# Performance work log

Hardware: AMD Instinct MI355X
Metric: run time of the kernel (lower is better)

The kernel has to match this reference:

```python
import jax, jax.numpy as jnp
from jax import lax
import numpy as np

EPS = 1e-5

def _bn(x, g, b):
    # training-mode BatchNorm2d: batch stats over (N, H, W), biased variance
    m = x.mean(axis=(0, 2, 3), keepdims=True)
    v = x.var(axis=(0, 2, 3), keepdims=True)
    return g[None, :, None, None] * (x - m) * lax.rsqrt(v + EPS) + b[None, :, None, None]

def _conv(x, w, b, stride, pad):
    y = lax.conv_general_dilated(x, w, (stride, stride), ((pad, pad), (pad, pad)),
                                 dimension_numbers=('NCHW', 'OIHW', 'NCHW'))
    return y + b[None, :, None, None]

def _convT(x, w, b):
    # torch ConvTranspose2d(k=4, stride=2, pad=1): equivalent to lhs-dilated conv
    # with spatially flipped kernel and padding k-1-pad = 2. w layout: (Cin, Cout, kh, kw)
    wf = jnp.transpose(w[:, :, ::-1, ::-1], (1, 0, 2, 3))  # -> (Cout, Cin, 4, 4)
    y = lax.conv_general_dilated(x, wf, (1, 1), ((2, 2), (2, 2)), lhs_dilation=(2, 2),
                                 dimension_numbers=('NCHW', 'OIHW', 'NCHW'))
    return y + b[None, :, None, None]

def setup_inputs() -> dict:
    key = jax.random.key(0)
    ks = jax.random.split(key, 8)
    s = 0.05
    inp = {
        'x':   jax.random.normal(ks[0], (32, 1, 256, 256), jnp.float32),
        'w1':  jax.random.normal(ks[1], (16, 1, 4, 4), jnp.float32) * s,
        'b1':  jnp.zeros((16,), jnp.float32),
        'g1':  jnp.ones((16,), jnp.float32),
        'be1': jnp.zeros((16,), jnp.float32),
        'w2':  jax.random.normal(ks[2], (32, 16, 4, 4), jnp.float32) * s,
        'b2':  jnp.zeros((32,), jnp.float32),
        'g2':  jnp.ones((32,), jnp.float32),
        'be2': jnp.zeros((32,), jnp.float32),
        'w3':  jax.random.normal(ks[3], (32, 32, 1, 1), jnp.float32) * s,
        'b3':  jnp.zeros((32,), jnp.float32),
        'g3':  jnp.ones((32,), jnp.float32),
        'be3': jnp.zeros((32,), jnp.float32),
        'emb': jax.random.normal(ks[4], (512, 32), jnp.float32) / 512.0,
        'dw1': jax.random.normal(ks[5], (32, 32, 1, 1), jnp.float32) * s,
        'db1': jnp.zeros((32,), jnp.float32),
        'dg1': jnp.ones((32,), jnp.float32),
        'dbe1': jnp.zeros((32,), jnp.float32),
        'dtw1': jax.random.normal(ks[6], (32, 16, 4, 4), jnp.float32) * s,
        'dtb1': jnp.zeros((16,), jnp.float32),
        'dg2': jnp.ones((16,), jnp.float32),
        'dbe2': jnp.zeros((16,), jnp.float32),
        'dtw2': jax.random.normal(ks[7], (16, 30, 4, 4), jnp.float32) * s,
        'dtb2': jnp.zeros((30,), jnp.float32),
    }
    return inp

def reference(x, w1, b1, g1, be1, w2, b2, g2, be2, w3, b3, g3, be3, emb,
              dw1, db1, dg1, dbe1, dtw1, dtb1, dg2, dbe2, dtw2, dtb2):
    # --- encoder ---
    h = jax.nn.relu(_bn(_conv(x, w1, b1, 2, 1), g1, be1))
    h = jax.nn.relu(_bn(_conv(h, w2, b2, 2, 1), g2, be2))
    z_e_x = _bn(_conv(h, w3, b3, 1, 0), g3, be3)            # (N, C, H, W)
    N, C, H, W = z_e_x.shape
    # --- VQ: matmul-based squared distance (same argmin as broadcast-subtract-sum) ---
    zt = jnp.transpose(z_e_x, (0, 2, 3, 1)).reshape(-1, C)  # (N*H*W, C)
    d = (jnp.sum(zt * zt, axis=1, keepdims=True)
         - 2.0 * zt @ emb.T
         + jnp.sum(emb * emb, axis=1)[None, :])             # (N*H*W, K)
    latents = jnp.argmin(d, axis=1).reshape(N, H, W)        # first-min index, like torch
    z_q_x = jnp.transpose(emb[latents], (0, 3, 1, 2))       # (N, C, H, W)
    # --- decoder ---
    h = jax.nn.relu(_bn(_conv(z_q_x, dw1, db1, 1, 0), dg1, dbe1))
    h = jax.nn.relu(_bn(_convT(h, dtw1, dtb1), dg2, dbe2))
    x_tilde = _convT(h, dtw2, dtb2)                          # (N, 30, 4H, 4W)
    return x_tilde, z_e_x, z_q_x, latents
```

## Files before the change

### kernel.cpp

```cpp
#include <hip/hip_runtime.h>
#include <hip/hip_bf16.h>

#define WS_SUMS  0
#define WS_W1T   4096
#define WS_W2T   8192
#define WS_W3T   40960
#define WS_DW1T  45056
#define WS_DT1T  49152
#define WS_DT2T  81920
#define WS_E2F   114688
#define WS_Y1    1048576
#define WS_Y5    1048576

#define SUM1 0
#define SUM2 512
#define SUM3 1024
#define SUM4 1536
#define SUM5 2048

#define OUT_XT 0
#define OUT_ZE 62914560
#define OUT_ZQ 67108864
#define OUT_LT 71303168

#define DO_Y2 0
#define DO_Y3 16777216
#define DO_Y4 33554432

__device__ __forceinline__ double ae9_wsumd(double v){
  #pragma unroll
  for (int off = 32; off; off >>= 1) v += __shfl_xor(v, off);
  return v;
}

template<int C>
__device__ __forceinline__ void ae9_statsf(const float* a, double* red, double* gsum){
  const int lane = threadIdx.x & 63, wid = threadIdx.x >> 6;
  #pragma unroll
  for (int c = 0; c < C; ++c){
    double av = (double)a[c];
    double s = ae9_wsumd(av);
    double q = ae9_wsumd(av*av);
    if (lane == 0){ red[(wid*C + c)*2] = s; red[(wid*C + c)*2 + 1] = q; }
  }
  __syncthreads();
  if ((int)threadIdx.x < C){
    double s = 0.0, q = 0.0;
    #pragma unroll
    for (int wv = 0; wv < 4; ++wv){ s += red[(wv*C + threadIdx.x)*2]; q += red[(wv*C + threadIdx.x)*2 + 1]; }
    atomicAdd(&gsum[2*threadIdx.x],     s);
    atomicAdd(&gsum[2*threadIdx.x + 1], q);
  }
}

template<int C>
__device__ __forceinline__ void ae9_statsf2(const float* a0, const float* a1, double* red, double* gsum){
  const int lane = threadIdx.x & 63, wid = threadIdx.x >> 6;
  #pragma unroll
  for (int c = 0; c < C; ++c){
    double v0 = (double)a0[c], v1 = (double)a1[c];
    double s = ae9_wsumd(v0 + v1);
    double q = ae9_wsumd(v0*v0 + v1*v1);
    if (lane == 0){ red[(wid*C + c)*2] = s; red[(wid*C + c)*2 + 1] = q; }
  }
  __syncthreads();
  if ((int)threadIdx.x < C){
    double s = 0.0, q = 0.0;
    #pragma unroll
    for (int wv = 0; wv < 4; ++wv){ s += red[(wv*C + threadIdx.x)*2]; q += red[(wv*C + threadIdx.x)*2 + 1]; }
    atomicAdd(&gsum[2*threadIdx.x],     s);
    atomicAdd(&gsum[2*threadIdx.x + 1], q);
  }
}

template<int C>
__device__ __forceinline__ void ae9_bnparams(float* pm, float* pr, float* pg, float* pb,
                                             const double* sums, const float* g, const float* be, double inv){
  if ((int)threadIdx.x < C){
    int c = threadIdx.x;
    double md = sums[2*c] * inv;
    double vd = sums[2*c+1] * inv - md*md;
    pm[c] = (float)md;
    float vf = (float)vd;
    pr[c] = __fdiv_rn(1.f, __fsqrt_rn(__fadd_rn(vf, 1e-5f)));
    pg[c] = g[c];
    pb[c] = be[c];
  }
  __syncthreads();
}

__device__ __forceinline__ float ae9_bn(float x, float m, float g, float r, float b){
  return __fadd_rn(__fmul_rn(__fmul_rn(g, __fsub_rn(x, m)), r), b);
}
__device__ __forceinline__ float ae9_bnrelu(float x, float m, float g, float r, float b){
  return fmaxf(ae9_bn(x, m, g, r, b), 0.f);
}

__device__ __forceinline__ float ae9_np_pairwise32(const float* a){
  float r[8];
  #pragma unroll
  for (int j = 0; j < 8; ++j)
    r[j] = __fadd_rn(__fadd_rn(__fadd_rn(a[j], a[8+j]), a[16+j]), a[24+j]);
  return __fadd_rn(__fadd_rn(__fadd_rn(r[0], r[1]), __fadd_rn(r[2], r[3])),
                   __fadd_rn(__fadd_rn(r[4], r[5]), __fadd_rn(r[6], r[7])));
}

__global__ void ae9_prep(const float* __restrict__ w1, const float* __restrict__ w2,
                         const float* __restrict__ w3, const float* __restrict__ dw1,
                         const float* __restrict__ dtw1, const float* __restrict__ dtw2,
                         const float* __restrict__ emb, char* __restrict__ wsb){
  const int t = threadIdx.x;
  float* w1T  = (float*)(wsb + WS_W1T);
  float* w2T  = (float*)(wsb + WS_W2T);
  float* w3T  = (float*)(wsb + WS_W3T);
  float* dw1T = (float*)(wsb + WS_DW1T);
  float* dt1T = (float*)(wsb + WS_DT1T);
  float* dt2T = (float*)(wsb + WS_DT2T);
  float* e2f  = (float*)(wsb + WS_E2F);
  if (t < 256) w1T[t] = w1[(t & 15)*16 + (t >> 4)];
  for (int i = t; i < 8192; i += 256){
    int co = i & 31, k = i >> 5;
    w2T[i] = w2[co*256 + k];
  }
  for (int i = t; i < 1024; i += 256){ int co = i & 31, ci = i >> 5; w3T[i]  = w3[co*32 + ci]; }
  for (int i = t; i < 1024; i += 256){ int co = i & 31, ci = i >> 5; dw1T[i] = dw1[co*32 + ci]; }
  for (int i = t; i < 8192; i += 256){
    int co = i & 15, ci = (i >> 4) & 31, tap = i >> 9;
    dt1T[i] = dtw1[(ci*16 + co)*16 + tap];
  }
  for (int i = t; i < 8192; i += 256){
    int co = i & 31; int r2 = i >> 5; int ci = r2 & 15; int tap = r2 >> 4;
    dt2T[i] = (co < 30) ? dtw2[(ci*30 + co)*16 + tap] : 0.f;
  }
  for (int k = t; k < 512; k += 256){
    float sq[32];
    #pragma unroll
    for (int c = 0; c < 32; ++c){ float e = emb[k*32 + c]; sq[c] = __fmul_rn(e, e); }
    e2f[k] = ae9_np_pairwise32(sq);
  }
}

__global__ void __launch_bounds__(256) ae9_conv1(const float* __restrict__ x, const float* __restrict__ w1T,
                         const float* __restrict__ b1, float* __restrict__ y1, double* __restrict__ sums1){
  __shared__ double red[4*16*2];
  const int idx = blockIdx.x*256 + threadIdx.x;
  const int ox = idx & 127, oy = (idx >> 7) & 127, n = idx >> 14;
  float acc[16];
  #pragma unroll
  for (int c = 0; c < 16; ++c) acc[c] = 0.f;
  const float* xp = x + n*65536;
  for (int ky = 0; ky < 4; ++ky){
    int iy = 2*oy - 1 + ky;
    if (iy < 0 || iy >= 256) continue;
    for (int kx = 0; kx < 4; ++kx){
      int ix = 2*ox - 1 + kx;
      if (ix < 0 || ix >= 256) continue;
      float v = xp[iy*256 + ix];
      const float* w = w1T + (ky*4 + kx)*16;
      #pragma unroll
      for (int c = 0; c < 16; ++c) acc[c] = __fmaf_rn(v, w[c], acc[c]);
    }
  }
  float yv[16];
  float* yp = y1 + n*262144 + oy*128 + ox;
  #pragma unroll
  for (int c = 0; c < 16; ++c){ yv[c] = __fadd_rn(acc[c], b1[c]); yp[c*16384] = yv[c]; }
  ae9_statsf<16>(yv, red, sums1);
}

__global__ void __launch_bounds__(256) ae9_conv2(const float* __restrict__ y1, const double* __restrict__ sums1,
                         const float* __restrict__ g1, const float* __restrict__ be1,
                         const float* __restrict__ w2T, const float* __restrict__ b2,
                         float* __restrict__ y2, double* __restrict__ sums2){
  __shared__ float pm[16], pr[16], pg[16], pb[16];
  __shared__ double red[4*32*2];
  ae9_bnparams<16>(pm, pr, pg, pb, sums1, g1, be1, 1.0/524288.0);
  const int idx = blockIdx.x*256 + threadIdx.x;
  const int ox = idx & 63, oy = (idx >> 6) & 63, n = idx >> 12;
  float acc[32];
  #pragma unroll
  for (int c = 0; c < 32; ++c) acc[c] = 0.f;
  const float* in = y1 + n*262144;
  for (int ci = 0; ci < 16; ++ci){
    const float m = pm[ci], g = pg[ci], r = pr[ci], b = pb[ci];
    const float* plane = in + ci*16384;
    for (int ky = 0; ky < 4; ++ky){
      int iy = 2*oy - 1 + ky;
      if (iy < 0 || iy >= 128) continue;
      for (int kx = 0; kx < 4; ++kx){
        int ix = 2*ox - 1 + kx;
        if (ix < 0 || ix >= 128) continue;
        float v = ae9_bnrelu(plane[iy*128 + ix], m, g, r, b);
        const float* w = w2T + (ci*16 + ky*4 + kx)*32;
        #pragma unroll
        for (int co = 0; co < 32; ++co) acc[co] = __fmaf_rn(v, w[co], acc[co]);
      }
    }
  }
  float yv[32];
  float* yp = y2 + n*131072 + oy*64 + ox;
  #pragma unroll
  for (int c = 0; c < 32; ++c){ yv[c] = __fadd_rn(acc[c], b2[c]); yp[c*4096] = yv[c]; }
  ae9_statsf<32>(yv, red, sums2);
}

__global__ void __launch_bounds__(256) ae9_conv3(const float* __restrict__ y2, const double* __restrict__ sums2,
                         const float* __restrict__ g2, const float* __restrict__ be2,
                         const float* __restrict__ w3T, const float* __restrict__ b3,
                         float* __restrict__ y3, double* __restrict__ sums3){
  __shared__ float pm[32], pr[32], pg[32], pb[32];
  __shared__ double red[4*32*2];
  ae9_bnparams<32>(pm, pr, pg, pb, sums2, g2, be2, 1.0/131072.0);
  const int idx = blockIdx.x*256 + threadIdx.x;
  const int sp = idx & 4095, n = idx >> 12;
  const float* in = y2 + n*131072 + sp;
  float acc[32];
  #pragma unroll
  for (int c = 0; c < 32; ++c) acc[c] = 0.f;
  for (int ci = 0; ci < 32; ++ci){
    float v = ae9_bnrelu(in[ci*4096], pm[ci], pg[ci], pr[ci], pb[ci]);
    const float* w = w3T + ci*32;
    #pragma unroll
    for (int co = 0; co < 32; ++co) acc[co] = __fmaf_rn(v, w[co], acc[co]);
  }
  float yv[32];
  float* yp = y3 + n*131072 + sp;
  #pragma unroll
  for (int c = 0; c < 32; ++c){ yv[c] = __fadd_rn(acc[c], b3[c]); yp[c*4096] = yv[c]; }
  ae9_statsf<32>(yv, red, sums3);
}

__global__ void __launch_bounds__(256) ae9_vq(const float* __restrict__ y3, const double* __restrict__ sums3,
                      const float* __restrict__ g3, const float* __restrict__ be3,
                      const float* __restrict__ emb, const float* __restrict__ e2f,
                      const float* __restrict__ dw1T, const float* __restrict__ db1,
                      float* __restrict__ y4, double* __restrict__ sums4,
                      float* __restrict__ out){
  __shared__ float pm[32], pr[32], pg[32], pb[32];
  __shared__ double red[4*32*2];
  ae9_bnparams<32>(pm, pr, pg, pb, sums3, g3, be3, 1.0/131072.0);
  const int idx = blockIdx.x*256 + threadIdx.x;
  const int sp = idx & 4095, n = idx >> 12;
  const float* in = y3 + n*131072 + sp;
  float zf[32], z2q[32], zf2[32];
  #pragma unroll
  for (int c = 0; c < 32; ++c){
    zf[c]  = ae9_bn(in[c*4096], pm[c], pg[c], pr[c], pb[c]);
    z2q[c] = __fmul_rn(zf[c], zf[c]);
    zf2[c] = __fmul_rn(2.0f, zf[c]);
  }
  float* ze = out + OUT_ZE + n*131072 + sp;
  #pragma unroll
  for (int c = 0; c < 32; ++c) ze[c*4096] = zf[c];
  const float z2 = ae9_np_pairwise32(z2q);
  float best = 3.4e38f; int bi = 0;
  for (int k = 0; k < 512; k += 8){
    float d8[8];
    #pragma unroll
    for (int j = 0; j < 8; ++j){
      const float* ek = emb + (k + j)*32;
      float acc = 0.f;
      #pragma unroll
      for (int c = 0; c < 32; ++c) acc = __fmaf_rn(zf2[c], ek[c], acc);
      float u = __fsub_rn(z2, acc);
      d8[j] = __fadd_rn(u, e2f[k + j]);
    }
    #pragma unroll
    for (int j = 0; j < 8; ++j)
      if (d8[j] < best){ best = d8[j]; bi = k + j; }
  }
  out[OUT_LT + idx] = (float)bi;
  const float4* er = reinterpret_cast<const float4*>(emb + bi*32);
  float* zq = out + OUT_ZQ + n*131072 + sp;
  float acc[32];
  #pragma unroll
  for (int c = 0; c < 32; ++c) acc[c] = db1[c];
  #pragma unroll
  for (int j = 0; j < 8; ++j){
    float4 f = er[j];
    zq[(4*j+0)*4096] = f.x;
    zq[(4*j+1)*4096] = f.y;
    zq[(4*j+2)*4096] = f.z;
    zq[(4*j+3)*4096] = f.w;
    const float* w0 = dw1T + (4*j + 0)*32;
    const float* w1 = dw1T + (4*j + 1)*32;
    const float* w2 = dw1T + (4*j + 2)*32;
    const float* w3 = dw1T + (4*j + 3)*32;
    #pragma unroll
    for (int co = 0; co < 32; ++co){
      acc[co] = fmaf(f.x, w0[co], acc[co]);
      acc[co] = fmaf(f.y, w1[co], acc[co]);
      acc[co] = fmaf(f.z, w2[co], acc[co]);
      acc[co] = fmaf(f.w, w3[co], acc[co]);
    }
  }
  float* yp = y4 + n*131072 + sp;
  #pragma unroll
  for (int c = 0; c < 32; ++c) yp[c*4096] = acc[c];
  ae9_statsf<32>(acc, red, sums4);
}

__global__ void __launch_bounds__(256) aeB_dect1(const float* __restrict__ y4, const double* __restrict__ sums4,
                         const float* __restrict__ g4, const float* __restrict__ be4,
                         const float* __restrict__ wT, const float* __restrict__ bias,
                         float* __restrict__ y5, double* __restrict__ sums5){
  __shared__ float pm[32], pr[32], pg[32], pb[32];
  __shared__ double red[4*16*2];
  ae9_bnparams<32>(pm, pr, pg, pb, sums4, g4, be4, 1.0/131072.0);
  const int w = __builtin_amdgcn_readfirstlane(blockIdx.x*4 + (threadIdx.x >> 6));
  const int j = threadIdx.x & 63;
  const int p = w & 1, oy = (w >> 1) & 127, n = w >> 8;
  const int ky0 = (oy & 1) ? 0 : 1;
  float acc[16];
  #pragma unroll
  for (int c = 0; c < 16; ++c) acc[c] = bias[c];
  const float* in = y4 + n*131072;
  for (int ci = 0; ci < 32; ++ci){
    const float m = pm[ci], g = pg[ci], r = pr[ci], b = pb[ci];
    const float* plane = in + ci*4096;
    #pragma unroll
    for (int ty = 0; ty < 2; ++ty){
      const int ky = ky0 + 2*ty;
      const int iy = (oy + 1 - ky) >> 1;
      if (iy < 0 || iy >= 64) continue;
      const float* row = plane + iy*64;
      #pragma unroll
      for (int tx = 0; tx < 2; ++tx){
        const int kx = p ? 2*tx : 1 + 2*tx;
        const float4* wv = reinterpret_cast<const float4*>(wT + ((ky*4 + kx)*32 + ci)*16);
        float wgt[16];
        #pragma unroll
        for (int q = 0; q < 4; ++q) reinterpret_cast<float4*>(wgt)[q] = wv[q];
        int ix = j + p - tx;
        float v = (ix >= 0 && ix < 64) ? ae9_bnrelu(row[ix], m, g, r, b) : 0.f;
        #pragma unroll
        for (int co = 0; co < 16; ++co) acc[co] = fmaf(v, wgt[co], acc[co]);
      }
    }
  }
  float* op = y5 + ((size_t)n*16)*16384 + oy*128 + p;
  #pragma unroll
  for (int co = 0; co < 16; ++co) op[co*16384 + 2*j] = acc[co];
  ae9_statsf<16>(acc, red, sums5);
}

__global__ void __launch_bounds__(256) aeB_dect2(const float* __restrict__ y5, const double* __restrict__ sums5,
                         const float* __restrict__ g5, const float* __restrict__ be5,
                         const float* __restrict__ wT, const float* __restrict__ bias,
                         float* __restrict__ out){
  __shared__ float pm[16], pr[16], pg[16], pb[16];
  ae9_bnparams<16>(pm, pr, pg, pb, sums5, g5, be5, 1.0/524288.0);
  const int w = __builtin_amdgcn_readfirstlane(blockIdx.x*4 + (threadIdx.x >> 6));
  const int j = threadIdx.x & 63;
  const int p = w & 1, oy = (w >> 1) & 255, n = w >> 9;
  const int ky0 = (oy & 1) ? 0 : 1;
  float a0[30], a1[30];
  #pragma unroll
  for (int c = 0; c < 30; ++c){ a0[c] = bias[c]; a1[c] = bias[c]; }
  const float* in = y5 + n*262144;
  for (int ci = 0; ci < 16; ++ci){
    const float m = pm[ci], g = pg[ci], r = pr[ci], b = pb[ci];
    const float* plane = in + ci*16384;
    #pragma unroll
    for (int ty = 0; ty < 2; ++ty){
      const int ky = ky0 + 2*ty;
      const int iy = (oy + 1 - ky) >> 1;
      if (iy < 0 || iy >= 128) continue;
      const float* row = plane + iy*128;
      #pragma unroll
      for (int tx = 0; tx < 2; ++tx){
        const int kx = p ? 2*tx : 1 + 2*tx;
        const float4* wv = reinterpret_cast<const float4*>(wT + ((ky*4 + kx)*16 + ci)*32);
        float wgt[32];
        #pragma unroll
        for (int q = 0; q < 8; ++q) reinterpret_cast<float4*>(wgt)[q] = wv[q];
        int ix0 = j + p - tx;
        int ix1 = ix0 + 64;
        float v0 = (ix0 >= 0 && ix0 < 128) ? ae9_bnrelu(row[ix0], m, g, r, b) : 0.f;
        float v1 = (ix1 >= 0 && ix1 < 128) ? ae9_bnrelu(row[ix1], m, g, r, b) : 0.f;
        #pragma unroll
        for (int co = 0; co < 30; ++co){
          a0[co] = fmaf(v0, wgt[co], a0[co]);
          a1[co] = fmaf(v1, wgt[co], a1[co]);
        }
      }
    }
  }
  float* op = out + OUT_XT + ((size_t)n*30)*65536 + oy*256 + p;
  #pragma unroll
  for (int co = 0; co < 30; ++co){
    op[co*65536 + 2*j]        = a0[co];
    op[co*65536 + 2*(j + 64)] = a1[co];
  }
}

extern "C" void kernel_launch(void* const* d_in, const int* in_sizes, int n_in,
                              void* d_out, int out_size, void* d_ws, size_t ws_size,
                              hipStream_t stream) {
  const float* x    = (const float*)d_in[0];
  const float* w1   = (const float*)d_in[1];
  const float* b1   = (const float*)d_in[2];
  const float* g1   = (const float*)d_in[3];
  const float* be1  = (const float*)d_in[4];
  const float* w2   = (const float*)d_in[5];
  const float* b2   = (const float*)d_in[6];
  const float* g2   = (const float*)d_in[7];
  const float* be2  = (const float*)d_in[8];
  const float* w3   = (const float*)d_in[9];
  const float* b3   = (const float*)d_in[10];
  const float* g3   = (const float*)d_in[11];
  const float* be3  = (const float*)d_in[12];
  const float* emb  = (const float*)d_in[13];
  const float* dw1  = (const float*)d_in[14];
  const float* db1  = (const float*)d_in[15];
  const float* dg1  = (const float*)d_in[16];
  const float* dbe1 = (const float*)d_in[17];
  const float* dtw1 = (const float*)d_in[18];
  const float* dtb1 = (const float*)d_in[19];
  const float* dg2  = (const float*)d_in[20];
  const float* dbe2 = (const float*)d_in[21];
  const float* dtw2 = (const float*)d_in[22];
  const float* dtb2 = (const float*)d_in[23];

  char* wsb = (char*)d_ws;
  char* ob  = (char*)d_out;
  float* out = (float*)d_out;

  double* sums1 = (double*)(wsb + WS_SUMS + SUM1);
  double* sums2 = (double*)(wsb + WS_SUMS + SUM2);
  double* sums3 = (double*)(wsb + WS_SUMS + SUM3);
  double* sums4 = (double*)(wsb + WS_SUMS + SUM4);
  double* sums5 = (double*)(wsb + WS_SUMS + SUM5);
  float* y1 = (float*)(wsb + WS_Y1);
  float* y5 = (float*)(wsb + WS_Y5);
  float* y2 = (float*)(ob + DO_Y2);
  float* y3 = (float*)(ob + DO_Y3);
  float* y4 = (float*)(ob + DO_Y4);

  (void)hipMemsetAsync(wsb + WS_SUMS, 0, 4096, stream);
  ae9_prep<<<1, 256, 0, stream>>>(w1, w2, w3, dw1, dtw1, dtw2, emb, wsb);
  ae9_conv1<<<2048, 256, 0, stream>>>(x, (const float*)(wsb + WS_W1T), b1, y1, sums1);
  ae9_conv2<<<512, 256, 0, stream>>>(y1, sums1, g1, be1, (const float*)(wsb + WS_W2T), b2, y2, sums2);
  ae9_conv3<<<512, 256, 0, stream>>>(y2, sums2, g2, be2, (const float*)(wsb + WS_W3T), b3, y3, sums3);
  ae9_vq<<<512, 256, 0, stream>>>(y3, sums3, g3, be3, emb, (const float*)(wsb + WS_E2F),
                                  (const float*)(wsb + WS_DW1T), db1, y4, sums4, out);
  aeB_dect1<<<2048, 256, 0, stream>>>(y4, sums4, dg1, dbe1, (const float*)(wsb + WS_DT1T), dtb1, y5, sums5);
  aeB_dect2<<<4096, 256, 0, stream>>>(y5, sums5, dg2, dbe2, (const float*)(wsb + WS_DT2T), dtb2, out);
}
```

Before: 699.9 us.

## Split VQ codebook search across four waves per pixel block

The VQ kernel now assigns each pixel to four threads (one per wave), each scanning a quarter of the 512 codebook entries, then reduces the partial argmins through shared memory. The grid grows fourfold (64 pixels per block) to expose more parallelism to the memory-latency-bound search. Ties resolve toward the lower index because waves are compared in order with strict less-than. The cost is that the BN loads and recompute are repeated in each of the four waves, and only wave 0 does the output and 1x1 conv work. The unused statsf2 helper is also removed.

```diff
diff --git a/kernel.cpp b/kernel.cpp
--- a/kernel.cpp
+++ b/kernel.cpp
@@ -41,26 +41,6 @@
     double av = (double)a[c];
     double s = ae9_wsumd(av);
     double q = ae9_wsumd(av*av);
-    if (lane == 0){ red[(wid*C + c)*2] = s; red[(wid*C + c)*2 + 1] = q; }
-  }
-  __syncthreads();
-  if ((int)threadIdx.x < C){
-    double s = 0.0, q = 0.0;
-    #pragma unroll
-    for (int wv = 0; wv < 4; ++wv){ s += red[(wv*C + threadIdx.x)*2]; q += red[(wv*C + threadIdx.x)*2 + 1]; }
-    atomicAdd(&gsum[2*threadIdx.x],     s);
-    atomicAdd(&gsum[2*threadIdx.x + 1], q);
-  }
-}
-
-template<int C>
-__device__ __forceinline__ void ae9_statsf2(const float* a0, const float* a1, double* red, double* gsum){
-  const int lane = threadIdx.x & 63, wid = threadIdx.x >> 6;
-  #pragma unroll
-  for (int c = 0; c < C; ++c){
-    double v0 = (double)a0[c], v1 = (double)a1[c];
-    double s = ae9_wsumd(v0 + v1);
-    double q = ae9_wsumd(v0*v0 + v1*v1);
     if (lane == 0){ red[(wid*C + c)*2] = s; red[(wid*C + c)*2 + 1] = q; }
   }
   __syncthreads();
@@ -230,7 +210,7 @@
   ae9_statsf<32>(yv, red, sums3);
 }
 
-__global__ void __launch_bounds__(256) ae9_vq(const float* __restrict__ y3, const double* __restrict__ sums3,
+__global__ void __launch_bounds__(256) aeC_vq(const float* __restrict__ y3, const double* __restrict__ sums3,
                       const float* __restrict__ g3, const float* __restrict__ be3,
                       const float* __restrict__ emb, const float* __restrict__ e2f,
                       const float* __restrict__ dw1T, const float* __restrict__ db1,
@@ -238,8 +218,13 @@
                       float* __restrict__ out){
   __shared__ float pm[32], pr[32], pg[32], pb[32];
   __shared__ double red[4*32*2];
+  __shared__ float dbest[256];
+  __shared__ int   bidx[256];
   ae9_bnparams<32>(pm, pr, pg, pb, sums3, g3, be3, 1.0/131072.0);
-  const int idx = blockIdx.x*256 + threadIdx.x;
+  const int tid = threadIdx.x;
+  const int pixL = tid & 63;
+  const int t = tid >> 6;
+  const int idx = blockIdx.x*64 + pixL;
   const int sp = idx & 4095, n = idx >> 12;
   const float* in = y3 + n*131072 + sp;
   float zf[32], z2q[32], zf2[32];
@@ -249,12 +234,10 @@
     z2q[c] = __fmul_rn(zf[c], zf[c]);
     zf2[c] = __fmul_rn(2.0f, zf[c]);
   }
-  float* ze = out + OUT_ZE + n*131072 + sp;
-  #pragma unroll
-  for (int c = 0; c < 32; ++c) ze[c*4096] = zf[c];
   const float z2 = ae9_np_pairwise32(z2q);
   float best = 3.4e38f; int bi = 0;
-  for (int k = 0; k < 512; k += 8){
+  const int k0 = t*128;
+  for (int k = k0; k < k0 + 128; k += 8){
     float d8[8];
     #pragma unroll
     for (int j = 0; j < 8; ++j){
@@ -269,35 +252,51 @@
     for (int j = 0; j < 8; ++j)
       if (d8[j] < best){ best = d8[j]; bi = k + j; }
   }
-  out[OUT_LT + idx] = (float)bi;
-  const float4* er = reinterpret_cast<const float4*>(emb + bi*32);
-  float* zq = out + OUT_ZQ + n*131072 + sp;
-  float acc[32];
-  #pragma unroll
-  for (int c = 0; c < 32; ++c) acc[c] = db1[c];
-  #pragma unroll
-  for (int j = 0; j < 8; ++j){
-    float4 f = er[j];
-    zq[(4*j+0)*4096] = f.x;
-    zq[(4*j+1)*4096] = f.y;
-    zq[(4*j+2)*4096] = f.z;
-    zq[(4*j+3)*4096] = f.w;
-    const float* w0 = dw1T + (4*j + 0)*32;
-    const float* w1 = dw1T + (4*j + 1)*32;
-    const float* w2 = dw1T + (4*j + 2)*32;
-    const float* w3 = dw1T + (4*j + 3)*32;
-    #pragma unroll
-    for (int co = 0; co < 32; ++co){
-      acc[co] = fmaf(f.x, w0[co], acc[co]);
-      acc[co] = fmaf(f.y, w1[co], acc[co]);
-      acc[co] = fmaf(f.z, w2[co], acc[co]);
-      acc[co] = fmaf(f.w, w3[co], acc[co]);
-    }
-  }
-  float* yp = y4 + n*131072 + sp;
-  #pragma unroll
-  for (int c = 0; c < 32; ++c) yp[c*4096] = acc[c];
-  ae9_statsf<32>(acc, red, sums4);
+  dbest[tid] = best; bidx[tid] = bi;
+  __syncthreads();
+  float y4acc[32];
+  if (t == 0){
+    float b0 = dbest[pixL]; int i0 = bidx[pixL];
+    #pragma unroll
+    for (int tt = 1; tt < 4; ++tt){
+      float bt = dbest[tt*64 + pixL];
+      if (bt < b0){ b0 = bt; i0 = bidx[tt*64 + pixL]; }
+    }
+    out[OUT_LT + idx] = (float)i0;
+    float* ze = out + OUT_ZE + n*131072 + sp;
+    #pragma unroll
+    for (int c = 0; c < 32; ++c) ze[c*4096] = zf[c];
+    const float4* er = reinterpret_cast<const float4*>(emb + i0*32);
+    float* zq = out + OUT_ZQ + n*131072 + sp;
+    #pragma unroll
+    for (int c = 0; c < 32; ++c) y4acc[c] = db1[c];
+    #pragma unroll
+    for (int j = 0; j < 8; ++j){
+      float4 f = er[j];
+      zq[(4*j+0)*4096] = f.x;
+      zq[(4*j+1)*4096] = f.y;
+      zq[(4*j+2)*4096] = f.z;
+      zq[(4*j+3)*4096] = f.w;
+      const float* w0 = dw1T + (4*j + 0)*32;
+      const float* w1 = dw1T + (4*j + 1)*32;
+      const float* w2 = dw1T + (4*j + 2)*32;
+      const float* w3 = dw1T + (4*j + 3)*32;
+      #pragma unroll
+      for (int co = 0; co < 32; ++co){
+        y4acc[co] = fmaf(f.x, w0[co], y4acc[co]);
+        y4acc[co] = fmaf(f.y, w1[co], y4acc[co]);
+        y4acc[co] = fmaf(f.z, w2[co], y4acc[co]);
+        y4acc[co] = fmaf(f.w, w3[co], y4acc[co]);
+      }
+    }
+    float* yp = y4 + n*131072 + sp;
+    #pragma unroll
+    for (int c = 0; c < 32; ++c) yp[c*4096] = y4acc[c];
+  } else {
+    #pragma unroll
+    for (int c = 0; c < 32; ++c) y4acc[c] = 0.f;
+  }
+  ae9_statsf<32>(y4acc, red, sums4);
 }
 
 __global__ void __launch_bounds__(256) aeB_dect1(const float* __restrict__ y4, const double* __restrict__ sums4,
@@ -442,8 +441,8 @@
   ae9_conv1<<<2048, 256, 0, stream>>>(x, (const float*)(wsb + WS_W1T), b1, y1, sums1);
   ae9_conv2<<<512, 256, 0, stream>>>(y1, sums1, g1, be1, (const float*)(wsb + WS_W2T), b2, y2, sums2);
   ae9_conv3<<<512, 256, 0, stream>>>(y2, sums2, g2, be2, (const float*)(wsb + WS_W3T), b3, y3, sums3);
-  ae9_vq<<<512, 256, 0, stream>>>(y3, sums3, g3, be3, emb, (const float*)(wsb + WS_E2F),
-                                  (const float*)(wsb + WS_DW1T), db1, y4, sums4, out);
+  aeC_vq<<<2048, 256, 0, stream>>>(y3, sums3, g3, be3, emb, (const float*)(wsb + WS_E2F),
+                                   (const float*)(wsb + WS_DW1T), db1, y4, sums4, out);
   aeB_dect1<<<2048, 256, 0, stream>>>(y4, sums4, dg1, dbe1, (const float*)(wsb + WS_DT1T), dtb1, y5, sums5);
   aeB_dect2<<<4096, 256, 0, stream>>>(y5, sums5, dg2, dbe2, (const float*)(wsb + WS_DT2T), dtb2, out);
 }
```

After: 870.5 us. +24.4%, slower.
